# Optimization experiments

Measured on AMD Instinct MI355X. Metric: run time of the kernel, lower is better.

## Reference

```python
import jax, jax.numpy as jnp
import numpy as np

P_DROP = 0.3
TEMP = 1.0
UNC_THRESH = 0.3
TOP_K = 2
EXTRA_K = 2  # min(2, num_experts - top_k)
NUM_SAMPLES = 5


def setup_inputs() -> dict:
    key = jax.random.key(0)
    ks = jax.random.split(key, 7)
    B, D, H, E = 16384, 4096, 128, 64
    return {
        "x": jax.random.normal(ks[0], (B, D), jnp.float32),
        "W1": jax.random.normal(ks[1], (D, H), jnp.float32) / np.sqrt(D),
        "b1": jnp.zeros((H,), jnp.float32),
        "W2": jax.random.normal(ks[2], (H, E), jnp.float32) / np.sqrt(H),
        "b2": jnp.zeros((E,), jnp.float32),
        "mask1_u": jax.random.uniform(ks[3], (NUM_SAMPLES, B, H), jnp.float32),
        "mask2_u": jax.random.uniform(ks[4], (NUM_SAMPLES, B, E), jnp.float32),
    }


def reference(x, W1, b1, W2, b2, mask1_u, mask2_u):
    scale = 1.0 / (1.0 - P_DROP)
    # layer1: Linear -> ReLU -> Dropout; W1 is shared, so compute once and
    # apply per-sample dropout masks (identical math to the torch loop).
    h = jax.nn.relu(x @ W1 + b1)                              # [B, H]
    h = h[None] * ((mask1_u >= P_DROP).astype(h.dtype) * scale)  # [S, B, H]
    # layer2: Linear -> Dropout
    logits = jnp.einsum("sbh,he->sbe", h, W2) + b2            # [S, B, E]
    logits = logits * ((mask2_u >= P_DROP).astype(logits.dtype) * scale)

    mean_logits = logits.mean(axis=0)                          # [B, E]
    probs = jax.nn.softmax(mean_logits / TEMP, axis=-1)        # [B, E]
    all_probs = jax.nn.softmax(logits / TEMP, axis=-1)         # [S, B, E]
    # torch .std() is unbiased (ddof=1)
    uncertainty = jnp.std(all_probs, axis=0, ddof=1).mean(axis=-1)  # [B]

    # top_k + conditional expansion by EXTRA_K when uncertain.
    full_probs, full_idx = jax.lax.top_k(probs, TOP_K + EXTRA_K)
    topk_probs, topk_idx = full_probs[:, :TOP_K], full_idx[:, :TOP_K]
    uncertain = (uncertainty > UNC_THRESH)[:, None]
    extra_probs = jnp.where(uncertain, full_probs[:, TOP_K:], 0.0)
    extra_idx = jnp.where(uncertain, full_idx[:, TOP_K:], -1)
    out_idx = jnp.concatenate([topk_idx, extra_idx], axis=1)       # [B, TOP_K+EXTRA_K]
    out_probs = jnp.concatenate([topk_probs, extra_probs], axis=1)
    return out_idx, out_probs, uncertainty
```

## Files before the change

### kernel.cpp

```cpp
#include <hip/hip_runtime.h>

typedef short short8 __attribute__((ext_vector_type(8)));
typedef short short4v __attribute__((ext_vector_type(4)));
typedef float f32x4 __attribute__((ext_vector_type(4)));

#define B_ROWS 16384
#define SCALE 1.4285714285714286f

__device__ __forceinline__ float bf2f(unsigned short u) {
    return __uint_as_float(((unsigned)u) << 16);
}
__device__ __forceinline__ unsigned short f2bf(float f) {
    unsigned u = __float_as_uint(f);
    u += 0x7fffu + ((u >> 16) & 1u);
    return (unsigned short)(u >> 16);
}

__device__ __forceinline__ void gl_lds16(const void* g, void* l) {
    __builtin_amdgcn_global_load_lds(
        (const __attribute__((address_space(1))) unsigned int*)g,
        (__attribute__((address_space(3))) unsigned int*)l, 16, 0, 0);
}

__device__ __forceinline__ float wave_max(float v) {
    #pragma unroll
    for (int m = 1; m < 64; m <<= 1) v = fmaxf(v, __shfl_xor(v, m, 64));
    return v;
}
__device__ __forceinline__ float wave_sum(float v) {
    #pragma unroll
    for (int m = 1; m < 64; m <<= 1) v += __shfl_xor(v, m, 64);
    return v;
}

__global__ void k_prep(const float* __restrict__ w1,
                       unsigned short* __restrict__ w1h,
                       unsigned short* __restrict__ w1l) {
    int tid = blockIdx.x * 256 + threadIdx.x;
    int n = tid >> 12, k = tid & 4095;
    float v = w1[k * 128 + n];
    unsigned short hi = f2bf(v);
    w1h[tid] = hi;
    w1l[tid] = f2bf(v - bf2f(hi));
}

__global__ __launch_bounds__(512, 4) void k_fused(
        const float* __restrict__ x,
        const unsigned short* __restrict__ w1h,
        const unsigned short* __restrict__ w1l,
        const float* __restrict__ b1,
        const float* __restrict__ w2,
        const float* __restrict__ b2,
        const float* __restrict__ m1,
        const float* __restrict__ m2,
        float* __restrict__ out) {
    __shared__ __attribute__((aligned(128))) char smem[81920];
    unsigned short* sAh0 = (unsigned short*)smem;
    unsigned short* sAl0 = (unsigned short*)(smem + 8192);
    unsigned short* sBh0 = (unsigned short*)(smem + 16384);
    unsigned short* sBl0 = (unsigned short*)(smem + 49152);
    float* hbuf = (float*)smem;
    float* hmb  = (float*)(smem + 16384);
    float* w2s  = (float*)(smem + 49152);
    float* lgs  = (float*)(smem + 16384);

    const int t = threadIdx.x;
    const int w = t >> 6, lane = t & 63;
    const int l15 = lane & 15, l4 = lane >> 4;
    const int rowBase = blockIdx.x << 5;

    const int am = t >> 4;
    const int rem = t & 15;
    const int aDst = (((am << 3) + ((rem >> 1) ^ (am & 7))) << 3) + ((rem & 1) << 2);

    f32x4 acc[2];
    #pragma unroll
    for (int mf = 0; mf < 2; ++mf) {
        f32x4 z = {0.f, 0.f, 0.f, 0.f};
        acc[mf] = z;
    }

    auto stageB = [&](int buf, int k0) {
        #pragma unroll
        for (int j = 0; j < 2; ++j) {
            int c = (j << 9) + t;
            int n = c >> 3;
            int cl = (c & 7) ^ (n & 7);
            const size_t go = (size_t)n * 4096 + k0 + (cl << 3);
            gl_lds16(w1h + go, sBh0 + (buf << 13) + (c << 3));
            gl_lds16(w1l + go, sBl0 + (buf << 13) + (c << 3));
        }
    };
    auto loadA = [&](int k0) {
        return *(const float4*)(x + ((size_t)(rowBase + am) << 12) + k0 + (rem << 2));
    };
    auto writeA = [&](int buf, float4 a0) {
        float av[4] = {a0.x, a0.y, a0.z, a0.w};
        short4v H, L;
        #pragma unroll
        for (int i = 0; i < 4; ++i) {
            unsigned short hi = f2bf(av[i]);
            H[i] = (short)hi;
            L[i] = (short)f2bf(av[i] - bf2f(hi));
        }
        *(short4v*)(sAh0 + (buf << 11) + aDst) = H;
        *(short4v*)(sAl0 + (buf << 11) + aDst) = L;
    };

    stageB(0, 0);
    writeA(0, loadA(0));
    __syncthreads();

    for (int it = 0; it < 64; ++it) {
        const int buf = it & 1;
        const bool pf = (it + 1 < 64);
        float4 aN = make_float4(0.f, 0.f, 0.f, 0.f);
        if (pf) {
            stageB(buf ^ 1, (it + 1) << 6);
            aN = loadA((it + 1) << 6);
        }
        #pragma unroll
        for (int ks = 0; ks < 2; ++ks) {
            short8 ah[2], al[2], bh, bl;
            #pragma unroll
            for (int mf = 0; mf < 2; ++mf) {
                int rm = (mf << 4) + l15;
                int pc = ((ks << 2) + l4) ^ (rm & 7);
                int o = ((rm << 3) + pc) << 3;
                ah[mf] = *(const short8*)(sAh0 + (buf << 11) + o);
                al[mf] = *(const short8*)(sAl0 + (buf << 11) + o);
            }
            {
                int rn = (w << 4) + l15;
                int pc = ((ks << 2) + l4) ^ (rn & 7);
                int o = ((rn << 3) + pc) << 3;
                bh = *(const short8*)(sBh0 + (buf << 13) + o);
                bl = *(const short8*)(sBl0 + (buf << 13) + o);
            }
            #pragma unroll
            for (int mf = 0; mf < 2; ++mf) {
                acc[mf] = __builtin_amdgcn_mfma_f32_16x16x32_bf16(ah[mf], bh, acc[mf], 0, 0, 0);
                acc[mf] = __builtin_amdgcn_mfma_f32_16x16x32_bf16(ah[mf], bl, acc[mf], 0, 0, 0);
                acc[mf] = __builtin_amdgcn_mfma_f32_16x16x32_bf16(al[mf], bh, acc[mf], 0, 0, 0);
            }
        }
        if (pf) writeA(buf ^ 1, aN);
        __syncthreads();
    }

    {
        const int col = (w << 4) + l15;
        const float bias = b1[col];
        #pragma unroll
        for (int mf = 0; mf < 2; ++mf) {
            const int rbase = (mf << 4) + (l4 << 2);
            #pragma unroll
            for (int rr = 0; rr < 4; ++rr) {
                const int r = rbase + rr;
                float v = acc[mf][rr] + bias;
                v = v > 0.f ? v : 0.f;
                hbuf[r * 128 + (col ^ ((r & 7) << 2))] = v;
            }
        }
    }
    __syncthreads();

    const int lr = t >> 4;
    const int eg = t & 15;
    const int e0 = eg << 2;
    const int row = rowBase + lr;
    const int lsw = (lr & 7) << 2;

    float acc2[5][4];
    #pragma unroll
    for (int s = 0; s < 5; ++s)
        #pragma unroll
        for (int e = 0; e < 4; ++e) acc2[s][e] = 0.f;

    auto stage_hm = [&](int slot, int sidx) {
        #pragma unroll
        for (int j = 0; j < 2; ++j) {
            int q = t + (j << 9);
            int r = q >> 5, kq = q & 31;
            float4 mu = *(const float4*)(m1 + (size_t)sidx * (B_ROWS * 128)
                                            + (((size_t)(rowBase + r)) << 7) + (kq << 2));
            int off = r * 128 + ((kq << 2) ^ ((r & 7) << 2));
            float4 h4 = *(const float4*)(hbuf + off);
            float4 hm4;
            hm4.x = (mu.x >= 0.3f) ? h4.x * SCALE : 0.f;
            hm4.y = (mu.y >= 0.3f) ? h4.y * SCALE : 0.f;
            hm4.z = (mu.z >= 0.3f) ? h4.z * SCALE : 0.f;
            hm4.w = (mu.w >= 0.3f) ? h4.w * SCALE : 0.f;
            *(float4*)(hmb + (slot << 12) + off) = hm4;
        }
    };

    #pragma unroll
    for (int j = 0; j < 4; ++j) {
        int q = t + (j << 9);
        *(float4*)(w2s + (q << 2)) = *(const float4*)(w2 + (q << 2));
    }
    stage_hm(0, 0);
    stage_hm(1, 1);
    __syncthreads();

    for (int p = 0; p < 3; ++p) {
        const int s0 = p << 1;
        const int ns = (p == 2) ? 1 : 2;
        const float* hm0 = hmb + lr * 128;
        const float* hm1 = hmb + 4096 + lr * 128;
        for (int kq = 0; kq < 32; ++kq) {
            const int hoff = (kq << 2) ^ lsw;
            float4 a0 = *(const float4*)(hm0 + hoff);
            float ha[4] = {a0.x, a0.y, a0.z, a0.w};
            float w2v[4][4];
            #pragma unroll
            for (int kk = 0; kk < 4; ++kk) {
                float4 wa = *(const float4*)(w2s + (((kq << 2) + kk) << 6) + e0);
                w2v[kk][0] = wa.x; w2v[kk][1] = wa.y; w2v[kk][2] = wa.z; w2v[kk][3] = wa.w;
            }
            #pragma unroll
            for (int kk = 0; kk < 4; ++kk)
                #pragma unroll
                for (int e = 0; e < 4; ++e)
                    acc2[s0][e] += ha[kk] * w2v[kk][e];
            if (ns == 2) {
                float4 a1 = *(const float4*)(hm1 + hoff);
                float hb[4] = {a1.x, a1.y, a1.z, a1.w};
                #pragma unroll
                for (int kk = 0; kk < 4; ++kk)
                    #pragma unroll
                    for (int e = 0; e < 4; ++e)
                        acc2[s0 + 1][e] += hb[kk] * w2v[kk][e];
            }
        }
        __syncthreads();
        if (p < 2) {
            stage_hm(0, (p << 1) + 2);
            if (p == 0) stage_hm(1, 3);
            __syncthreads();
        }
    }

    {
        float4 ba = *(const float4*)(b2 + e0);
        float bv4[4] = {ba.x, ba.y, ba.z, ba.w};
        #pragma unroll
        for (int s = 0; s < 5; ++s) {
            const float* m2p = m2 + ((size_t)s * B_ROWS + row) * 64 + e0;
            float4 ma = *(const float4*)m2p;
            float mk[4] = {ma.x, ma.y, ma.z, ma.w};
            float lv[4];
            #pragma unroll
            for (int e = 0; e < 4; ++e) {
                float v = acc2[s][e] + bv4[e];
                lv[e] = (mk[e] >= 0.3f) ? v * SCALE : 0.f;
            }
            *(float4*)(lgs + ((s << 5) + lr) * 64 + e0) =
                make_float4(lv[0], lv[1], lv[2], lv[3]);
        }
    }
    __syncthreads();

    for (int r4 = 0; r4 < 4; ++r4) {
        const int r = (w << 2) + r4;
        float l[5], p[5];
        #pragma unroll
        for (int s = 0; s < 5; ++s)
            l[s] = lgs[((s << 5) + r) * 64 + lane];

        float ml = ((((l[0] + l[1]) + l[2]) + l[3]) + l[4]) / 5.0f;

        #pragma unroll
        for (int s = 0; s < 5; ++s) {
            float mx = wave_max(l[s]);
            float ev = expf(l[s] - mx);
            float sm = wave_sum(ev);
            p[s] = ev / sm;
        }

        float mx = wave_max(ml);
        float ev = expf(ml - mx);
        float sm = wave_sum(ev);
        float prob = ev / sm;

        float mean = ((((p[0] + p[1]) + p[2]) + p[3]) + p[4]) / 5.0f;
        float var = 0.f;
        #pragma unroll
        for (int s = 0; s < 5; ++s) { float d = p[s] - mean; var += d * d; }
        float sd = sqrtf(var * 0.25f);
        float unc = wave_sum(sd) / 64.0f;

        float pv = prob;
        float vv[4]; int vi[4];
        #pragma unroll
        for (int q = 0; q < 4; ++q) {
            float bvx = pv; int bi = lane;
            #pragma unroll
            for (int m = 1; m < 64; m <<= 1) {
                float ov = __shfl_xor(bvx, m, 64);
                int oi = __shfl_xor(bi, m, 64);
                if (ov > bvx || (ov == bvx && oi < bi)) { bvx = ov; bi = oi; }
            }
            vv[q] = bvx; vi[q] = bi;
            if (lane == bi) pv = -1.f;
        }

        if (lane == 0) {
            int grow = rowBase + r;
            bool ug = unc > 0.3f;
            float4 fi = make_float4((float)vi[0], (float)vi[1],
                                    ug ? (float)vi[2] : -1.f,
                                    ug ? (float)vi[3] : -1.f);
            *(float4*)(out + (size_t)grow * 4) = fi;
            float4 fp = make_float4(vv[0], vv[1],
                                    ug ? vv[2] : 0.f,
                                    ug ? vv[3] : 0.f);
            *(float4*)(out + 65536 + (size_t)grow * 4) = fp;
            out[131072 + grow] = unc;
        }
    }
}

extern "C" void kernel_launch(void* const* d_in, const int* in_sizes, int n_in,
                              void* d_out, int out_size, void* d_ws, size_t ws_size,
                              hipStream_t stream) {
    const float* x  = (const float*)d_in[0];
    const float* W1 = (const float*)d_in[1];
    const float* b1 = (const float*)d_in[2];
    const float* W2 = (const float*)d_in[3];
    const float* b2 = (const float*)d_in[4];
    const float* m1 = (const float*)d_in[5];
    const float* m2 = (const float*)d_in[6];
    float* out = (float*)d_out;
    char* ws = (char*)d_ws;

    unsigned short* w1h = (unsigned short*)ws;
    unsigned short* w1l = (unsigned short*)(ws + (1 << 20));

    k_prep <<<2048, 256, 0, stream>>>(W1, w1h, w1l);
    k_fused<<<512,  512, 0, stream>>>(x, w1h, w1l, b1, W2, b2, m1, m2, out);
}
```

Before: 470.1 us.

## Double row tile to 64 per block with 2x2 MFMA fragments per wave

Each block now handles 64 rows instead of 32, and each wave computes a 32x32 tile (2x2 MFMA fragments) instead of 32x16. Each staged W1 tile is reused across twice as many rows, which halves W1 global/LDS traffic per row and halves the grid to 256 blocks. The cost is 128KB of LDS per block and an occupancy hint lowered to 2. With 256 CUs this leaves about one block per CU and less latency hiding.

```diff
diff --git a/kernel.cpp b/kernel.cpp
--- a/kernel.cpp
+++ b/kernel.cpp
@@ -1,7 +1,6 @@
 #include <hip/hip_runtime.h>
 
 typedef short short8 __attribute__((ext_vector_type(8)));
-typedef short short4v __attribute__((ext_vector_type(4)));
 typedef float f32x4 __attribute__((ext_vector_type(4)));
 
 #define B_ROWS 16384
@@ -44,7 +43,7 @@
     w1l[tid] = f2bf(v - bf2f(hi));
 }
 
-__global__ __launch_bounds__(512, 4) void k_fused(
+__global__ __launch_bounds__(512, 2) void k_fused(
         const float* __restrict__ x,
         const unsigned short* __restrict__ w1h,
         const unsigned short* __restrict__ w1l,
@@ -54,31 +53,34 @@
         const float* __restrict__ m1,
         const float* __restrict__ m2,
         float* __restrict__ out) {
-    __shared__ __attribute__((aligned(128))) char smem[81920];
+    __shared__ __attribute__((aligned(128))) char smem[131072];
     unsigned short* sAh0 = (unsigned short*)smem;
-    unsigned short* sAl0 = (unsigned short*)(smem + 8192);
-    unsigned short* sBh0 = (unsigned short*)(smem + 16384);
-    unsigned short* sBl0 = (unsigned short*)(smem + 49152);
+    unsigned short* sAl0 = (unsigned short*)(smem + 16384);
+    unsigned short* sBh0 = (unsigned short*)(smem + 32768);
+    unsigned short* sBl0 = (unsigned short*)(smem + 65536);
     float* hbuf = (float*)smem;
-    float* hmb  = (float*)(smem + 16384);
-    float* w2s  = (float*)(smem + 49152);
-    float* lgs  = (float*)(smem + 16384);
+    float* hmb  = (float*)(smem + 32768);
+    float* w2s  = (float*)(smem + 98304);
+    float* lgs  = (float*)(smem + 32768);
 
     const int t = threadIdx.x;
     const int w = t >> 6, lane = t & 63;
     const int l15 = lane & 15, l4 = lane >> 4;
-    const int rowBase = blockIdx.x << 5;
-
-    const int am = t >> 4;
-    const int rem = t & 15;
-    const int aDst = (((am << 3) + ((rem >> 1) ^ (am & 7))) << 3) + ((rem & 1) << 2);
-
-    f32x4 acc[2];
-    #pragma unroll
-    for (int mf = 0; mf < 2; ++mf) {
-        f32x4 z = {0.f, 0.f, 0.f, 0.f};
-        acc[mf] = z;
-    }
+    const int cg = w & 3, rg = w >> 2;
+    const int rowBase = blockIdx.x << 6;
+
+    const int am = t >> 3;
+    const int rem = t & 7;
+    const int aDst = ((am << 3) + (rem ^ (am & 7))) << 3;
+
+    f32x4 acc[2][2];
+    #pragma unroll
+    for (int mf = 0; mf < 2; ++mf)
+        #pragma unroll
+        for (int nf = 0; nf < 2; ++nf) {
+            f32x4 z = {0.f, 0.f, 0.f, 0.f};
+            acc[mf][nf] = z;
+        }
 
     auto stageB = [&](int buf, int k0) {
         #pragma unroll
@@ -91,95 +93,109 @@
             gl_lds16(w1l + go, sBl0 + (buf << 13) + (c << 3));
         }
     };
-    auto loadA = [&](int k0) {
-        return *(const float4*)(x + ((size_t)(rowBase + am) << 12) + k0 + (rem << 2));
-    };
-    auto writeA = [&](int buf, float4 a0) {
-        float av[4] = {a0.x, a0.y, a0.z, a0.w};
-        short4v H, L;
-        #pragma unroll
-        for (int i = 0; i < 4; ++i) {
+    auto loadA0 = [&](int k0) {
+        return *(const float4*)(x + ((size_t)(rowBase + am) << 12) + k0 + (rem << 3));
+    };
+    auto loadA1 = [&](int k0) {
+        return *(const float4*)(x + ((size_t)(rowBase + am) << 12) + k0 + (rem << 3) + 4);
+    };
+    auto writeA = [&](int buf, float4 a0, float4 a1) {
+        float av[8] = {a0.x, a0.y, a0.z, a0.w, a1.x, a1.y, a1.z, a1.w};
+        short8 H, L;
+        #pragma unroll
+        for (int i = 0; i < 8; ++i) {
             unsigned short hi = f2bf(av[i]);
             H[i] = (short)hi;
             L[i] = (short)f2bf(av[i] - bf2f(hi));
         }
-        *(short4v*)(sAh0 + (buf << 11) + aDst) = H;
-        *(short4v*)(sAl0 + (buf << 11) + aDst) = L;
+        *(short8*)(sAh0 + (buf << 12) + aDst) = H;
+        *(short8*)(sAl0 + (buf << 12) + aDst) = L;
     };
 
     stageB(0, 0);
-    writeA(0, loadA(0));
+    writeA(0, loadA0(0), loadA1(0));
     __syncthreads();
 
     for (int it = 0; it < 64; ++it) {
         const int buf = it & 1;
         const bool pf = (it + 1 < 64);
-        float4 aN = make_float4(0.f, 0.f, 0.f, 0.f);
+        float4 aN0 = make_float4(0.f, 0.f, 0.f, 0.f);
+        float4 aN1 = make_float4(0.f, 0.f, 0.f, 0.f);
         if (pf) {
             stageB(buf ^ 1, (it + 1) << 6);
-            aN = loadA((it + 1) << 6);
+            aN0 = loadA0((it + 1) << 6);
+            aN1 = loadA1((it + 1) << 6);
         }
         #pragma unroll
         for (int ks = 0; ks < 2; ++ks) {
-            short8 ah[2], al[2], bh, bl;
+            short8 ah[2], al[2], bh[2], bl[2];
             #pragma unroll
             for (int mf = 0; mf < 2; ++mf) {
-                int rm = (mf << 4) + l15;
+                int rm = (rg << 5) + (mf << 4) + l15;
                 int pc = ((ks << 2) + l4) ^ (rm & 7);
                 int o = ((rm << 3) + pc) << 3;
-                ah[mf] = *(const short8*)(sAh0 + (buf << 11) + o);
-                al[mf] = *(const short8*)(sAl0 + (buf << 11) + o);
-            }
-            {
-                int rn = (w << 4) + l15;
+                ah[mf] = *(const short8*)(sAh0 + (buf << 12) + o);
+                al[mf] = *(const short8*)(sAl0 + (buf << 12) + o);
+            }
+            #pragma unroll
+            for (int nf = 0; nf < 2; ++nf) {
+                int rn = (cg << 5) + (nf << 4) + l15;
                 int pc = ((ks << 2) + l4) ^ (rn & 7);
                 int o = ((rn << 3) + pc) << 3;
-                bh = *(const short8*)(sBh0 + (buf << 13) + o);
-                bl = *(const short8*)(sBl0 + (buf << 13) + o);
-            }
+                bh[nf] = *(const short8*)(sBh0 + (buf << 13) + o);
+                bl[nf] = *(const short8*)(sBl0 + (buf << 13) + o);
+            }
+            #pragma unroll
+            for (int mf = 0; mf < 2; ++mf)
+                #pragma unroll
+                for (int nf = 0; nf < 2; ++nf) {
+                    acc[mf][nf] = __builtin_amdgcn_mfma_f32_16x16x32_bf16(
+                        ah[mf], bh[nf], acc[mf][nf], 0, 0, 0);
+                    acc[mf][nf] = __builtin_amdgcn_mfma_f32_16x16x32_bf16(
+                        ah[mf], bl[nf], acc[mf][nf], 0, 0, 0);
+                    acc[mf][nf] = __builtin_amdgcn_mfma_f32_16x16x32_bf16(
+                        al[mf], bh[nf], acc[mf][nf], 0, 0, 0);
+                }
+        }
+        if (pf) writeA(buf ^ 1, aN0, aN1);
+        __syncthreads();
+    }
+
+    {
+        #pragma unroll
+        for (int nf = 0; nf < 2; ++nf) {
+            const int col = (cg << 5) + (nf << 4) + l15;
+            const float bias = b1[col];
             #pragma unroll
             for (int mf = 0; mf < 2; ++mf) {
-                acc[mf] = __builtin_amdgcn_mfma_f32_16x16x32_bf16(ah[mf], bh, acc[mf], 0, 0, 0);
-                acc[mf] = __builtin_amdgcn_mfma_f32_16x16x32_bf16(ah[mf], bl, acc[mf], 0, 0, 0);
-                acc[mf] = __builtin_amdgcn_mfma_f32_16x16x32_bf16(al[mf], bh, acc[mf], 0, 0, 0);
-            }
-        }
-        if (pf) writeA(buf ^ 1, aN);
-        __syncthreads();
-    }
-
-    {
-        const int col = (w << 4) + l15;
-        const float bias = b1[col];
-        #pragma unroll
-        for (int mf = 0; mf < 2; ++mf) {
-            const int rbase = (mf << 4) + (l4 << 2);
-            #pragma unroll
-            for (int rr = 0; rr < 4; ++rr) {
-                const int r = rbase + rr;
-                float v = acc[mf][rr] + bias;
-                v = v > 0.f ? v : 0.f;
-                hbuf[r * 128 + (col ^ ((r & 7) << 2))] = v;
+                const int rbase = (rg << 5) + (mf << 4) + (l4 << 2);
+                #pragma unroll
+                for (int rr = 0; rr < 4; ++rr) {
+                    const int r = rbase + rr;
+                    float v = acc[mf][nf][rr] + bias;
+                    v = v > 0.f ? v : 0.f;
+                    hbuf[r * 128 + (col ^ ((r & 7) << 2))] = v;
+                }
             }
         }
     }
     __syncthreads();
 
-    const int lr = t >> 4;
-    const int eg = t & 15;
-    const int e0 = eg << 2;
+    const int lr = t >> 3;
+    const int eg = t & 7;
+    const int e0 = eg << 3;
     const int row = rowBase + lr;
     const int lsw = (lr & 7) << 2;
 
-    float acc2[5][4];
+    float acc2[5][8];
     #pragma unroll
     for (int s = 0; s < 5; ++s)
         #pragma unroll
-        for (int e = 0; e < 4; ++e) acc2[s][e] = 0.f;
+        for (int e = 0; e < 8; ++e) acc2[s][e] = 0.f;
 
     auto stage_hm = [&](int slot, int sidx) {
         #pragma unroll
-        for (int j = 0; j < 2; ++j) {
+        for (int j = 0; j < 4; ++j) {
             int q = t + (j << 9);
             int r = q >> 5, kq = q & 31;
             float4 mu = *(const float4*)(m1 + (size_t)sidx * (B_ROWS * 128)
@@ -191,7 +207,7 @@
             hm4.y = (mu.y >= 0.3f) ? h4.y * SCALE : 0.f;
             hm4.z = (mu.z >= 0.3f) ? h4.z * SCALE : 0.f;
             hm4.w = (mu.w >= 0.3f) ? h4.w * SCALE : 0.f;
-            *(float4*)(hmb + (slot << 12) + off) = hm4;
+            *(float4*)(hmb + (slot << 13) + off) = hm4;
         }
     };
 
@@ -208,21 +224,23 @@
         const int s0 = p << 1;
         const int ns = (p == 2) ? 1 : 2;
         const float* hm0 = hmb + lr * 128;
-        const float* hm1 = hmb + 4096 + lr * 128;
+        const float* hm1 = hmb + 8192 + lr * 128;
         for (int kq = 0; kq < 32; ++kq) {
             const int hoff = (kq << 2) ^ lsw;
             float4 a0 = *(const float4*)(hm0 + hoff);
             float ha[4] = {a0.x, a0.y, a0.z, a0.w};
-            float w2v[4][4];
+            float w2v[4][8];
             #pragma unroll
             for (int kk = 0; kk < 4; ++kk) {
                 float4 wa = *(const float4*)(w2s + (((kq << 2) + kk) << 6) + e0);
+                float4 wb = *(const float4*)(w2s + (((kq << 2) + kk) << 6) + e0 + 4);
                 w2v[kk][0] = wa.x; w2v[kk][1] = wa.y; w2v[kk][2] = wa.z; w2v[kk][3] = wa.w;
+                w2v[kk][4] = wb.x; w2v[kk][5] = wb.y; w2v[kk][6] = wb.z; w2v[kk][7] = wb.w;
             }
             #pragma unroll
             for (int kk = 0; kk < 4; ++kk)
                 #pragma unroll
-                for (int e = 0; e < 4; ++e)
+                for (int e = 0; e < 8; ++e)
                     acc2[s0][e] += ha[kk] * w2v[kk][e];
             if (ns == 2) {
                 float4 a1 = *(const float4*)(hm1 + hoff);
@@ -230,7 +248,7 @@
                 #pragma unroll
                 for (int kk = 0; kk < 4; ++kk)
                     #pragma unroll
-                    for (int e = 0; e < 4; ++e)
+                    for (int e = 0; e < 8; ++e)
                         acc2[s0 + 1][e] += hb[kk] * w2v[kk][e];
             }
         }
@@ -244,30 +262,33 @@
 
     {
         float4 ba = *(const float4*)(b2 + e0);
-        float bv4[4] = {ba.x, ba.y, ba.z, ba.w};
+        float4 bb = *(const float4*)(b2 + e0 + 4);
+        float bv[8] = {ba.x, ba.y, ba.z, ba.w, bb.x, bb.y, bb.z, bb.w};
         #pragma unroll
         for (int s = 0; s < 5; ++s) {
             const float* m2p = m2 + ((size_t)s * B_ROWS + row) * 64 + e0;
             float4 ma = *(const float4*)m2p;
-            float mk[4] = {ma.x, ma.y, ma.z, ma.w};
-            float lv[4];
-            #pragma unroll
-            for (int e = 0; e < 4; ++e) {
-                float v = acc2[s][e] + bv4[e];
+            float4 mb = *(const float4*)(m2p + 4);
+            float mk[8] = {ma.x, ma.y, ma.z, ma.w, mb.x, mb.y, mb.z, mb.w};
+            float lv[8];
+            #pragma unroll
+            for (int e = 0; e < 8; ++e) {
+                float v = acc2[s][e] + bv[e];
                 lv[e] = (mk[e] >= 0.3f) ? v * SCALE : 0.f;
             }
-            *(float4*)(lgs + ((s << 5) + lr) * 64 + e0) =
-                make_float4(lv[0], lv[1], lv[2], lv[3]);
+            float* dst = lgs + ((s << 6) + lr) * 64 + e0;
+            *(float4*)dst = make_float4(lv[0], lv[1], lv[2], lv[3]);
+            *(float4*)(dst + 4) = make_float4(lv[4], lv[5], lv[6], lv[7]);
         }
     }
     __syncthreads();
 
-    for (int r4 = 0; r4 < 4; ++r4) {
-        const int r = (w << 2) + r4;
+    for (int r8 = 0; r8 < 8; ++r8) {
+        const int r = (w << 3) + r8;
         float l[5], p[5];
         #pragma unroll
         for (int s = 0; s < 5; ++s)
-            l[s] = lgs[((s << 5) + r) * 64 + lane];
+            l[s] = lgs[((s << 6) + r) * 64 + lane];
 
         float ml = ((((l[0] + l[1]) + l[2]) + l[3]) + l[4]) / 5.0f;
 
@@ -339,5 +360,5 @@
     unsigned short* w1l = (unsigned short*)(ws + (1 << 20));
 
     k_prep <<<2048, 256, 0, stream>>>(W1, w1h, w1l);
-    k_fused<<<512,  512, 0, stream>>>(x, w1h, w1l, b1, W2, b2, m1, m2, out);
-}
+    k_fused<<<256,  512, 0, stream>>>(x, w1h, w1l, b1, W2, b2, m1, m2, out);
+}
```

Result: slower. 484.4 us (+3.0%).

## Split fused kernel into 64-row GEMM and separate logits/stats kernel

Applied to the files above, without the earlier changes.

The fused kernel is split in two. A GEMM kernel with 64-row tiles arranged as a 2x2 wave grid reuses each W1 tile across twice as many rows and uses a triple-buffered B ring with a lighter barrier. It writes the ReLU hidden activations to a global workspace, and a second kernel reads them back for the dropout, logits and uncertainty stage. The larger tiles halve the W1 restaging traffic per row and decouple the occupancy of the two phases. The cost is a global round-trip of the 8 MB hidden tensor and an extra launch, while the GEMM runs only 256 blocks at one block per CU.

```diff
diff --git a/kernel.cpp b/kernel.cpp
--- a/kernel.cpp
+++ b/kernel.cpp
@@ -1,7 +1,6 @@
 #include <hip/hip_runtime.h>
 
 typedef short short8 __attribute__((ext_vector_type(8)));
-typedef short short4v __attribute__((ext_vector_type(4)));
 typedef float f32x4 __attribute__((ext_vector_type(4)));
 
 #define B_ROWS 16384
@@ -44,130 +43,172 @@
     w1l[tid] = f2bf(v - bf2f(hi));
 }
 
-__global__ __launch_bounds__(512, 4) void k_fused(
+struct A2 { float4 a, b; };
+
+__global__ __launch_bounds__(512, 1) void k_gemm(
         const float* __restrict__ x,
         const unsigned short* __restrict__ w1h,
         const unsigned short* __restrict__ w1l,
         const float* __restrict__ b1,
+        float* __restrict__ hout) {
+    __shared__ __attribute__((aligned(128))) char smem[131072];
+    unsigned short* sBh0 = (unsigned short*)smem;
+    unsigned short* sBl0 = (unsigned short*)(smem + 49152);
+    unsigned short* sAh0 = (unsigned short*)(smem + 98304);
+    unsigned short* sAl0 = (unsigned short*)(smem + 114688);
+
+    const int t = threadIdx.x;
+    const int w = t >> 6, lane = t & 63;
+    const int l15 = lane & 15, l4 = lane >> 4;
+    const int cg = w & 3, rg = w >> 2;
+    const int rowBase = blockIdx.x << 6;
+
+    const int am = t >> 3;
+    const int rem = t & 7;
+    const int aDst = ((am << 3) + (rem ^ (am & 7))) << 3;
+
+    f32x4 acc[2][2];
+    #pragma unroll
+    for (int mf = 0; mf < 2; ++mf)
+        #pragma unroll
+        for (int nf = 0; nf < 2; ++nf) {
+            f32x4 z = {0.f, 0.f, 0.f, 0.f};
+            acc[mf][nf] = z;
+        }
+
+    auto stageB = [&](int bbuf, int k0) {
+        #pragma unroll
+        for (int j = 0; j < 2; ++j) {
+            int c = (j << 9) + t;
+            int n = c >> 3;
+            int cl = (c & 7) ^ (n & 7);
+            const size_t go = (size_t)n * 4096 + k0 + (cl << 3);
+            gl_lds16(w1h + go, sBh0 + (bbuf << 13) + (c << 3));
+            gl_lds16(w1l + go, sBl0 + (bbuf << 13) + (c << 3));
+        }
+    };
+    auto loadA = [&](int k0) {
+        const float* src = x + ((size_t)(rowBase + am) << 12) + k0 + (rem << 3);
+        A2 r;
+        r.a = *(const float4*)src;
+        r.b = *(const float4*)(src + 4);
+        return r;
+    };
+    auto writeA = [&](int abuf, A2 v) {
+        float av[8] = {v.a.x, v.a.y, v.a.z, v.a.w, v.b.x, v.b.y, v.b.z, v.b.w};
+        short8 H, L;
+        #pragma unroll
+        for (int i = 0; i < 8; ++i) {
+            unsigned short hi = f2bf(av[i]);
+            H[i] = (short)hi;
+            L[i] = (short)f2bf(av[i] - bf2f(hi));
+        }
+        *(short8*)(sAh0 + (abuf << 12) + aDst) = H;
+        *(short8*)(sAl0 + (abuf << 12) + aDst) = L;
+    };
+    auto compute = [&](int abuf, int bbuf) {
+        #pragma unroll
+        for (int ks = 0; ks < 2; ++ks) {
+            short8 ah[2], al[2], bh[2], bl[2];
+            #pragma unroll
+            for (int mf = 0; mf < 2; ++mf) {
+                int rm = (rg << 5) + (mf << 4) + l15;
+                int pc = ((ks << 2) + l4) ^ (rm & 7);
+                int o = ((rm << 3) + pc) << 3;
+                ah[mf] = *(const short8*)(sAh0 + (abuf << 12) + o);
+                al[mf] = *(const short8*)(sAl0 + (abuf << 12) + o);
+            }
+            #pragma unroll
+            for (int nf = 0; nf < 2; ++nf) {
+                int rn = (cg << 5) + (nf << 4) + l15;
+                int pc = ((ks << 2) + l4) ^ (rn & 7);
+                int o = ((rn << 3) + pc) << 3;
+                bh[nf] = *(const short8*)(sBh0 + (bbuf << 13) + o);
+                bl[nf] = *(const short8*)(sBl0 + (bbuf << 13) + o);
+            }
+            #pragma unroll
+            for (int mf = 0; mf < 2; ++mf)
+                #pragma unroll
+                for (int nf = 0; nf < 2; ++nf) {
+                    acc[mf][nf] = __builtin_amdgcn_mfma_f32_16x16x32_bf16(
+                        ah[mf], bh[nf], acc[mf][nf], 0, 0, 0);
+                    acc[mf][nf] = __builtin_amdgcn_mfma_f32_16x16x32_bf16(
+                        ah[mf], bl[nf], acc[mf][nf], 0, 0, 0);
+                    acc[mf][nf] = __builtin_amdgcn_mfma_f32_16x16x32_bf16(
+                        al[mf], bh[nf], acc[mf][nf], 0, 0, 0);
+                }
+        }
+    };
+    #define SOFTBAR() do { \
+        asm volatile("s_waitcnt lgkmcnt(0)" ::: "memory"); \
+        __builtin_amdgcn_s_barrier(); } while (0)
+
+    int rb0 = 0, rb1 = 1, rb2 = 2;
+    stageB(0, 0);
+    stageB(1, 64);
+    A2 P = loadA(0);
+    A2 Q = loadA(64);
+    writeA(0, P);
+    __syncthreads();
+
+    for (int m = 0; m < 31; ++m) {
+        const int kE = (2 * m + 2) << 6;
+        const int kO = (2 * m + 3) << 6;
+        stageB(rb2, kE);
+        P = loadA(kE);
+        writeA(1, Q);
+        compute(0, rb0);
+        SOFTBAR();
+        { int tb = rb0; rb0 = rb1; rb1 = rb2; rb2 = tb; }
+        stageB(rb2, kO);
+        Q = loadA(kO);
+        writeA(0, P);
+        compute(1, rb0);
+        SOFTBAR();
+        { int tb = rb0; rb0 = rb1; rb1 = rb2; rb2 = tb; }
+    }
+    writeA(1, Q);
+    compute(0, rb0);
+    SOFTBAR();
+    { int tb = rb0; rb0 = rb1; rb1 = rb2; rb2 = tb; }
+    compute(1, rb0);
+
+    #pragma unroll
+    for (int nf = 0; nf < 2; ++nf) {
+        const int col = (cg << 5) + (nf << 4) + l15;
+        const float bias = b1[col];
+        #pragma unroll
+        for (int mf = 0; mf < 2; ++mf) {
+            const int rbase = (rg << 5) + (mf << 4) + (l4 << 2);
+            #pragma unroll
+            for (int rr = 0; rr < 4; ++rr) {
+                const int r = rowBase + rbase + rr;
+                float v = acc[mf][nf][rr] + bias;
+                hout[(size_t)r * 128 + col] = v > 0.f ? v : 0.f;
+            }
+        }
+    }
+    #undef SOFTBAR
+}
+
+__global__ __launch_bounds__(512, 2) void k_logstats(
+        const float* __restrict__ hg,
         const float* __restrict__ w2,
         const float* __restrict__ b2,
         const float* __restrict__ m1,
         const float* __restrict__ m2,
         float* __restrict__ out) {
-    __shared__ __attribute__((aligned(128))) char smem[81920];
-    unsigned short* sAh0 = (unsigned short*)smem;
-    unsigned short* sAl0 = (unsigned short*)(smem + 8192);
-    unsigned short* sBh0 = (unsigned short*)(smem + 16384);
-    unsigned short* sBl0 = (unsigned short*)(smem + 49152);
-    float* hbuf = (float*)smem;
-    float* hmb  = (float*)(smem + 16384);
-    float* w2s  = (float*)(smem + 49152);
-    float* lgs  = (float*)(smem + 16384);
+    __shared__ __attribute__((aligned(128))) char smem[65536];
+    float* hmb = (float*)smem;
+    float* w2s = (float*)(smem + 32768);
+    float* lgs = (float*)smem;
 
     const int t = threadIdx.x;
     const int w = t >> 6, lane = t & 63;
-    const int l15 = lane & 15, l4 = lane >> 4;
-    const int rowBase = blockIdx.x << 5;
-
-    const int am = t >> 4;
-    const int rem = t & 15;
-    const int aDst = (((am << 3) + ((rem >> 1) ^ (am & 7))) << 3) + ((rem & 1) << 2);
-
-    f32x4 acc[2];
-    #pragma unroll
-    for (int mf = 0; mf < 2; ++mf) {
-        f32x4 z = {0.f, 0.f, 0.f, 0.f};
-        acc[mf] = z;
-    }
-
-    auto stageB = [&](int buf, int k0) {
-        #pragma unroll
-        for (int j = 0; j < 2; ++j) {
-            int c = (j << 9) + t;
-            int n = c >> 3;
-            int cl = (c & 7) ^ (n & 7);
-            const size_t go = (size_t)n * 4096 + k0 + (cl << 3);
-            gl_lds16(w1h + go, sBh0 + (buf << 13) + (c << 3));
-            gl_lds16(w1l + go, sBl0 + (buf << 13) + (c << 3));
-        }
-    };
-    auto loadA = [&](int k0) {
-        return *(const float4*)(x + ((size_t)(rowBase + am) << 12) + k0 + (rem << 2));
-    };
-    auto writeA = [&](int buf, float4 a0) {
-        float av[4] = {a0.x, a0.y, a0.z, a0.w};
-        short4v H, L;
-        #pragma unroll
-        for (int i = 0; i < 4; ++i) {
-            unsigned short hi = f2bf(av[i]);
-            H[i] = (short)hi;
-            L[i] = (short)f2bf(av[i] - bf2f(hi));
-        }
-        *(short4v*)(sAh0 + (buf << 11) + aDst) = H;
-        *(short4v*)(sAl0 + (buf << 11) + aDst) = L;
-    };
-
-    stageB(0, 0);
-    writeA(0, loadA(0));
-    __syncthreads();
-
-    for (int it = 0; it < 64; ++it) {
-        const int buf = it & 1;
-        const bool pf = (it + 1 < 64);
-        float4 aN = make_float4(0.f, 0.f, 0.f, 0.f);
-        if (pf) {
-            stageB(buf ^ 1, (it + 1) << 6);
-            aN = loadA((it + 1) << 6);
-        }
-        #pragma unroll
-        for (int ks = 0; ks < 2; ++ks) {
-            short8 ah[2], al[2], bh, bl;
-            #pragma unroll
-            for (int mf = 0; mf < 2; ++mf) {
-                int rm = (mf << 4) + l15;
-                int pc = ((ks << 2) + l4) ^ (rm & 7);
-                int o = ((rm << 3) + pc) << 3;
-                ah[mf] = *(const short8*)(sAh0 + (buf << 11) + o);
-                al[mf] = *(const short8*)(sAl0 + (buf << 11) + o);
-            }
-            {
-                int rn = (w << 4) + l15;
-                int pc = ((ks << 2) + l4) ^ (rn & 7);
-                int o = ((rn << 3) + pc) << 3;
-                bh = *(const short8*)(sBh0 + (buf << 13) + o);
-                bl = *(const short8*)(sBl0 + (buf << 13) + o);
-            }
-            #pragma unroll
-            for (int mf = 0; mf < 2; ++mf) {
-                acc[mf] = __builtin_amdgcn_mfma_f32_16x16x32_bf16(ah[mf], bh, acc[mf], 0, 0, 0);
-                acc[mf] = __builtin_amdgcn_mfma_f32_16x16x32_bf16(ah[mf], bl, acc[mf], 0, 0, 0);
-                acc[mf] = __builtin_amdgcn_mfma_f32_16x16x32_bf16(al[mf], bh, acc[mf], 0, 0, 0);
-            }
-        }
-        if (pf) writeA(buf ^ 1, aN);
-        __syncthreads();
-    }
-
-    {
-        const int col = (w << 4) + l15;
-        const float bias = b1[col];
-        #pragma unroll
-        for (int mf = 0; mf < 2; ++mf) {
-            const int rbase = (mf << 4) + (l4 << 2);
-            #pragma unroll
-            for (int rr = 0; rr < 4; ++rr) {
-                const int r = rbase + rr;
-                float v = acc[mf][rr] + bias;
-                v = v > 0.f ? v : 0.f;
-                hbuf[r * 128 + (col ^ ((r & 7) << 2))] = v;
-            }
-        }
-    }
-    __syncthreads();
-
     const int lr = t >> 4;
     const int eg = t & 15;
     const int e0 = eg << 2;
+    const int rowBase = blockIdx.x << 5;
     const int row = rowBase + lr;
     const int lsw = (lr & 7) << 2;
 
@@ -182,16 +223,16 @@
         for (int j = 0; j < 2; ++j) {
             int q = t + (j << 9);
             int r = q >> 5, kq = q & 31;
+            size_t gidx = ((size_t)(rowBase + r)) << 7;
             float4 mu = *(const float4*)(m1 + (size_t)sidx * (B_ROWS * 128)
-                                            + (((size_t)(rowBase + r)) << 7) + (kq << 2));
-            int off = r * 128 + ((kq << 2) ^ ((r & 7) << 2));
-            float4 h4 = *(const float4*)(hbuf + off);
+                                            + gidx + (kq << 2));
+            float4 h4 = *(const float4*)(hg + gidx + (kq << 2));
             float4 hm4;
             hm4.x = (mu.x >= 0.3f) ? h4.x * SCALE : 0.f;
             hm4.y = (mu.y >= 0.3f) ? h4.y * SCALE : 0.f;
             hm4.z = (mu.z >= 0.3f) ? h4.z * SCALE : 0.f;
             hm4.w = (mu.w >= 0.3f) ? h4.w * SCALE : 0.f;
-            *(float4*)(hmb + (slot << 12) + off) = hm4;
+            *(float4*)(hmb + (slot << 12) + r * 128 + ((kq << 2) ^ ((r & 7) << 2))) = hm4;
         }
     };
 
@@ -337,7 +378,9 @@
 
     unsigned short* w1h = (unsigned short*)ws;
     unsigned short* w1l = (unsigned short*)(ws + (1 << 20));
-
-    k_prep <<<2048, 256, 0, stream>>>(W1, w1h, w1l);
-    k_fused<<<512,  512, 0, stream>>>(x, w1h, w1l, b1, W2, b2, m1, m2, out);
-}
+    float* h = (float*)(ws + (2 << 20));
+
+    k_prep    <<<2048, 256, 0, stream>>>(W1, w1h, w1l);
+    k_gemm    <<<256,  512, 0, stream>>>(x, w1h, w1l, b1, h);
+    k_logstats<<<512,  512, 0, stream>>>(h, W2, b2, m1, m2, out);
+}
```

Result: slower. 483.1 us (+2.8%).
